# Kernel tuning notes

Measured on AMD Instinct MI355X. Metric: run time of the kernel, lower is better.

The kernel has to match this reference:

```python
import jax, jax.numpy as jnp
import numpy as np

N = 40000
E = 640000
D_IN = 128
D_OUT = 128
K = 3
LAMBDA_MAX = 2.0
LN_EPS = 1e-5


def setup_inputs() -> dict:
    key = jax.random.key(0)
    k1, k2, k3, k4, k5 = jax.random.split(key, 5)
    x = jax.random.normal(k1, (N, D_IN), dtype=jnp.float32)
    edge_index = jax.random.randint(k2, (2, E), 0, N, dtype=jnp.int64)
    edge_weight = jax.random.uniform(k3, (E,), dtype=jnp.float32)
    # Chebyshev weights: one [D_IN, D_OUT] matrix per hop k, plus shared bias
    W = jax.random.normal(k4, (K, D_IN, D_OUT), dtype=jnp.float32) / np.sqrt(D_IN)
    bias = jnp.zeros((D_OUT,), dtype=jnp.float32)
    gamma = jnp.ones((D_OUT,), dtype=jnp.float32)
    beta = jnp.zeros((D_OUT,), dtype=jnp.float32)
    return {"x": x, "edge_weight": edge_weight, "W": W, "bias": bias,
            "gamma": gamma, "beta": beta, "edge_index": edge_index}


def reference(x, edge_weight, W, bias, gamma, beta, edge_index):
    row, col = edge_index[0], edge_index[1]

    # Symmetric normalization of the graph Laplacian (PyG ChebConv, norm='sym')
    deg = jax.ops.segment_sum(edge_weight, row, num_segments=N)
    dinv = jnp.where(deg > 0, jax.lax.rsqrt(deg), 0.0)
    # scaled Laplacian L_hat = (2/lambda_max) * (I - A_norm) - I
    # off-diagonal entries: -(2/lambda_max) * a_norm ; diagonal: 2/lambda_max - 1
    scale = 2.0 / LAMBDA_MAX
    norm = -scale * dinv[row] * edge_weight * dinv[col]  # [E]
    diag = scale - 1.0  # == 0 for lambda_max = 2

    def prop(h):  # L_hat @ h via gather / scale / scatter-add
        msg = norm[:, None] * h[col]                      # [E, D]
        return jax.ops.segment_sum(msg, row, num_segments=N) + diag * h

    # Chebyshev recursion: T0 = x, T1 = L_hat x, Tk = 2 L_hat T_{k-1} - T_{k-2}
    Tx0 = x
    out = Tx0 @ W[0]
    Tx1 = prop(x)
    out = out + Tx1 @ W[1]
    for k in range(2, K):
        Tx2 = 2.0 * prop(Tx1) - Tx0
        out = out + Tx2 @ W[k]
        Tx0, Tx1 = Tx1, Tx2
    out = out + bias

    # LayerNorm over channels + ReLU
    mean = jnp.mean(out, axis=-1, keepdims=True)
    var = jnp.var(out, axis=-1, keepdims=True)
    out = (out - mean) * jax.lax.rsqrt(var + LN_EPS) * gamma + beta
    return jax.nn.relu(out)
```

## Files before the change

### kernel.cpp

```cpp
#include <hip/hip_runtime.h>

#define NN 40000
#define EE 640000
#define DD 128
#define CAP 96

typedef __attribute__((ext_vector_type(8))) __bf16 bf16x8;
typedef __attribute__((ext_vector_type(4))) float f32x4;
typedef unsigned long long ull;

static __device__ __forceinline__ unsigned short bfs(float f) {
    __bf16 h = (__bf16)f;
    return __builtin_bit_cast(unsigned short, h);
}
static __device__ __forceinline__ float blo(unsigned int v) {
    return __builtin_bit_cast(float, v << 16);
}
static __device__ __forceinline__ float bhi(unsigned int v) {
    return __builtin_bit_cast(float, v & 0xffff0000u);
}

__global__ __launch_bounds__(256) void k_pre(const int* __restrict__ ei,
                                             const float* __restrict__ ew,
                                             const float* __restrict__ x,
                                             const float* __restrict__ W,
                                             ull* __restrict__ degcnt,
                                             int2* __restrict__ pair,
                                             unsigned short* __restrict__ xb,
                                             unsigned short* __restrict__ Wt) {
    int b = blockIdx.x;
    int tid = threadIdx.x;
    if (b < 2500) {
        int e = b * 256 + tid;
        int r = ei[e];
        int c = ei[EE + e];
        float w = ew[e];
        unsigned int q = __float2uint_rn(w * 16777216.0f);
        ull old = atomicAdd(degcnt + r, (1ULL << 32) | (ull)q);
        int rk = (int)(old >> 32);
        if (rk < CAP)
            pair[(size_t)r * CAP + rk] = make_int2(c, __float_as_int(w));
    } else if (b < 3125) {
        int base = (b - 2500) * 2048 + tid;
        #pragma unroll
        for (int it = 0; it < 8; it++) {
            int i = base + it * 256;
            float4 v = ((const float4*)x)[i];
            ushort4 p;
            p.x = bfs(v.x); p.y = bfs(v.y); p.z = bfs(v.z); p.w = bfs(v.w);
            ((ushort4*)xb)[i] = p;
        }
    } else {
        int t = (b - 3125) * 256 + tid;
        int n = t / 384;
        int c = t - n * 384;
        Wt[t] = bfs(W[(size_t)c * 128 + n]);
    }
}

__global__ __launch_bounds__(256) void k_dinv(const ull* __restrict__ degcnt,
                                              float* __restrict__ dinv) {
    int i = blockIdx.x * 256 + threadIdx.x;
    if (i < NN) {
        unsigned int lo = (unsigned int)degcnt[i];
        dinv[i] = lo > 0 ? rsqrtf((float)lo * (1.0f / 16777216.0f)) : 0.0f;
    }
}

__global__ __launch_bounds__(256) void k_prop(const ull* __restrict__ degcnt,
                                              const int2* __restrict__ pair,
                                              const unsigned short* __restrict__ hb,
                                              const float* __restrict__ dinv,
                                              const unsigned short* __restrict__ subb,
                                              float alpha, float betac,
                                              unsigned short* __restrict__ outb) {
    int grp = (blockIdx.x * 256 + threadIdx.x) >> 4;
    int q = threadIdx.x & 15;

    ull dc = degcnt[grp];
    int cnt = (int)(dc >> 32);
    if (cnt > CAP) cnt = CAP;
    unsigned int lo = (unsigned int)dc;
    float dr = lo > 0 ? rsqrtf((float)lo * (1.0f / 16777216.0f)) : 0.0f;

    int s = grp * CAP, t = s + cnt;
    float a0 = 0.f, a1 = 0.f, a2 = 0.f, a3 = 0.f, a4 = 0.f, a5 = 0.f, a6 = 0.f, a7 = 0.f;

    int e = s;
    for (; e + 4 <= t; e += 4) {
        int2 p0 = pair[e + 0];
        int2 p1 = pair[e + 1];
        int2 p2 = pair[e + 2];
        int2 p3 = pair[e + 3];
        uint4 h0 = *(const uint4*)(hb + (size_t)p0.x * DD + q * 8);
        uint4 h1 = *(const uint4*)(hb + (size_t)p1.x * DD + q * 8);
        uint4 h2 = *(const uint4*)(hb + (size_t)p2.x * DD + q * 8);
        uint4 h3 = *(const uint4*)(hb + (size_t)p3.x * DD + q * 8);
        float n0 = __int_as_float(p0.y) * dinv[p0.x];
        float n1 = __int_as_float(p1.y) * dinv[p1.x];
        float n2 = __int_as_float(p2.y) * dinv[p2.x];
        float n3 = __int_as_float(p3.y) * dinv[p3.x];
        a0 = fmaf(n0, blo(h0.x), a0); a1 = fmaf(n0, bhi(h0.x), a1);
        a2 = fmaf(n0, blo(h0.y), a2); a3 = fmaf(n0, bhi(h0.y), a3);
        a4 = fmaf(n0, blo(h0.z), a4); a5 = fmaf(n0, bhi(h0.z), a5);
        a6 = fmaf(n0, blo(h0.w), a6); a7 = fmaf(n0, bhi(h0.w), a7);
        a0 = fmaf(n1, blo(h1.x), a0); a1 = fmaf(n1, bhi(h1.x), a1);
        a2 = fmaf(n1, blo(h1.y), a2); a3 = fmaf(n1, bhi(h1.y), a3);
        a4 = fmaf(n1, blo(h1.z), a4); a5 = fmaf(n1, bhi(h1.z), a5);
        a6 = fmaf(n1, blo(h1.w), a6); a7 = fmaf(n1, bhi(h1.w), a7);
        a0 = fmaf(n2, blo(h2.x), a0); a1 = fmaf(n2, bhi(h2.x), a1);
        a2 = fmaf(n2, blo(h2.y), a2); a3 = fmaf(n2, bhi(h2.y), a3);
        a4 = fmaf(n2, blo(h2.z), a4); a5 = fmaf(n2, bhi(h2.z), a5);
        a6 = fmaf(n2, blo(h2.w), a6); a7 = fmaf(n2, bhi(h2.w), a7);
        a0 = fmaf(n3, blo(h3.x), a0); a1 = fmaf(n3, bhi(h3.x), a1);
        a2 = fmaf(n3, blo(h3.y), a2); a3 = fmaf(n3, bhi(h3.y), a3);
        a4 = fmaf(n3, blo(h3.z), a4); a5 = fmaf(n3, bhi(h3.z), a5);
        a6 = fmaf(n3, blo(h3.w), a6); a7 = fmaf(n3, bhi(h3.w), a7);
    }
    for (; e < t; e++) {
        int2 pr = pair[e];
        float nv = __int_as_float(pr.y) * dinv[pr.x];
        uint4 hv = *(const uint4*)(hb + (size_t)pr.x * DD + q * 8);
        a0 = fmaf(nv, blo(hv.x), a0); a1 = fmaf(nv, bhi(hv.x), a1);
        a2 = fmaf(nv, blo(hv.y), a2); a3 = fmaf(nv, bhi(hv.y), a3);
        a4 = fmaf(nv, blo(hv.z), a4); a5 = fmaf(nv, bhi(hv.z), a5);
        a6 = fmaf(nv, blo(hv.w), a6); a7 = fmaf(nv, bhi(hv.w), a7);
    }

    float scale = -alpha * dr;
    if (subb != nullptr) {
        const unsigned short* sp = subb + (size_t)grp * DD + q * 8;
        uint4 sv = *(const uint4*)sp;
        a0 = fmaf(scale, a0, betac * blo(sv.x));
        a1 = fmaf(scale, a1, betac * bhi(sv.x));
        a2 = fmaf(scale, a2, betac * blo(sv.y));
        a3 = fmaf(scale, a3, betac * bhi(sv.y));
        a4 = fmaf(scale, a4, betac * blo(sv.z));
        a5 = fmaf(scale, a5, betac * bhi(sv.z));
        a6 = fmaf(scale, a6, betac * blo(sv.w));
        a7 = fmaf(scale, a7, betac * bhi(sv.w));
    } else {
        a0 *= scale; a1 *= scale; a2 *= scale; a3 *= scale;
        a4 *= scale; a5 *= scale; a6 *= scale; a7 *= scale;
    }
    ushort4 o0, o1;
    o0.x = bfs(a0); o0.y = bfs(a1); o0.z = bfs(a2); o0.w = bfs(a3);
    o1.x = bfs(a4); o1.y = bfs(a5); o1.z = bfs(a6); o1.w = bfs(a7);
    unsigned short* op = outb + (size_t)grp * DD + q * 8;
    *(ushort4*)(op) = o0;
    *(ushort4*)(op + 4) = o1;
}

__global__ __launch_bounds__(256) void k_gemm_mfma_ln(
        const unsigned short* __restrict__ xb, const unsigned short* __restrict__ t1b,
        const unsigned short* __restrict__ t2b, const unsigned short* __restrict__ Wt,
        const float* __restrict__ bias, const float* __restrict__ gamma,
        const float* __restrict__ beta, float* __restrict__ out) {
    int tid = threadIdx.x;
    int lane = tid & 63;
    int wv = tid >> 6;
    int quad = lane >> 4;
    int l15 = lane & 15;
    int rowq = blockIdx.x * 128 + wv * 32;

    int r0 = rowq + l15;       if (r0 > NN - 1) r0 = NN - 1;
    int r1 = rowq + 16 + l15;  if (r1 > NN - 1) r1 = NN - 1;

    float bias_l[8], gamma_l[8], beta_l[8];
    #pragma unroll
    for (int nt = 0; nt < 8; nt++) {
        int cc = nt * 16 + l15;
        bias_l[nt] = bias[cc];
        gamma_l[nt] = gamma[cc];
        beta_l[nt] = beta[cc];
    }

    f32x4 acc[2][8];
    #pragma unroll
    for (int mt = 0; mt < 2; mt++)
        #pragma unroll
        for (int nt = 0; nt < 8; nt++)
            acc[mt][nt] = (f32x4){0.f, 0.f, 0.f, 0.f};

    #pragma unroll
    for (int c = 0; c < 12; c++) {
        const unsigned short* src = (c < 4) ? xb : ((c < 8) ? t1b : t2b);
        int kk = (c & 3) * 32 + quad * 8;
        bf16x8 a0 = *(const bf16x8*)(src + (size_t)r0 * DD + kk);
        bf16x8 a1 = *(const bf16x8*)(src + (size_t)r1 * DD + kk);
        #pragma unroll
        for (int nt = 0; nt < 8; nt++) {
            bf16x8 b = *(const bf16x8*)(Wt + (size_t)(nt * 16 + l15) * 384 + c * 32 + quad * 8);
            acc[0][nt] = __builtin_amdgcn_mfma_f32_16x16x32_bf16(a0, b, acc[0][nt], 0, 0, 0);
            acc[1][nt] = __builtin_amdgcn_mfma_f32_16x16x32_bf16(a1, b, acc[1][nt], 0, 0, 0);
        }
    }

    #pragma unroll
    for (int mt = 0; mt < 2; mt++) {
        #pragma unroll
        for (int reg = 0; reg < 4; reg++) {
            float v[8];
            float s = 0.f, sq = 0.f;
            #pragma unroll
            for (int nt = 0; nt < 8; nt++) {
                v[nt] = acc[mt][nt][reg] + bias_l[nt];
                s += v[nt];
                sq += v[nt] * v[nt];
            }
            #pragma unroll
            for (int m = 1; m <= 8; m <<= 1) {
                s  += __shfl_xor(s, m, 64);
                sq += __shfl_xor(sq, m, 64);
            }
            float mean = s * (1.0f / 128.0f);
            float var = sq * (1.0f / 128.0f) - mean * mean;
            float inv = rsqrtf(var + 1e-5f);
            int grow = rowq + mt * 16 + quad * 4 + reg;
            if (grow < NN) {
                #pragma unroll
                for (int nt = 0; nt < 8; nt++) {
                    float o = fmaxf((v[nt] - mean) * inv * gamma_l[nt] + beta_l[nt], 0.0f);
                    out[(size_t)grow * DD + nt * 16 + l15] = o;
                }
            }
        }
    }
}

extern "C" void kernel_launch(void* const* d_in, const int* in_sizes, int n_in,
                              void* d_out, int out_size, void* d_ws, size_t ws_size,
                              hipStream_t stream) {
    const float* x     = (const float*)d_in[0];
    const float* ew    = (const float*)d_in[1];
    const float* W     = (const float*)d_in[2];
    const float* bias  = (const float*)d_in[3];
    const float* gamma = (const float*)d_in[4];
    const float* beta  = (const float*)d_in[5];
    const int*   ei    = (const int*)d_in[6];
    float* out = (float*)d_out;

    char* ws = (char*)d_ws;
    size_t o = 0;
    auto alloc = [&](size_t bytes) { void* p = ws + o; o += (bytes + 255) & ~(size_t)255; return p; };
    ull*   degcnt = (ull*) alloc((size_t)NN * 8);
    float* dinv  = (float*)alloc((size_t)NN * 4);
    int2*  pair  = (int2*) alloc((size_t)NN * CAP * 8);
    unsigned short* xb  = (unsigned short*)alloc((size_t)NN * DD * 2);
    unsigned short* t1b = (unsigned short*)alloc((size_t)NN * DD * 2);
    unsigned short* t2b = (unsigned short*)alloc((size_t)NN * DD * 2);
    unsigned short* Wt  = (unsigned short*)alloc((size_t)384 * 128 * 2);

    hipMemsetAsync(degcnt, 0, (size_t)NN * 8, stream);

    k_pre<<<3317, 256, 0, stream>>>(ei, ew, x, W, degcnt, pair, xb, Wt);
    k_dinv<<<(NN + 255) / 256, 256, 0, stream>>>(degcnt, dinv);

    k_prop<<<NN / 16, 256, 0, stream>>>(degcnt, pair, xb, dinv, nullptr, 1.0f, 0.0f, t1b);
    k_prop<<<NN / 16, 256, 0, stream>>>(degcnt, pair, t1b, dinv, xb, 2.0f, -1.0f, t2b);

    k_gemm_mfma_ln<<<(NN + 127) / 128, 256, 0, stream>>>(xb, t1b, t2b, Wt, bias, gamma, beta, out);
}
```

Before: 206.0 us.

## Fuse dinv into propagation, batch tail edges, retile GEMM to 160-row blocks

Drops the separate dinv kernel and its buffer. Each propagation step now recomputes rsqrt of the neighbour degree from degcnt on the fly, which removes one launch but does an 8-byte load plus an rsqrt per edge. The scalar remainder loop becomes a single masked batch of three edges, so the gathers can be issued together. The GEMM+LayerNorm kernel uses 5 waves per block over 250 blocks, which divides 40000 rows exactly, so the clamping and bounds checks are removed.

```diff
diff --git a/kernel.cpp b/kernel.cpp
--- a/kernel.cpp
+++ b/kernel.cpp
@@ -18,6 +18,10 @@
 }
 static __device__ __forceinline__ float bhi(unsigned int v) {
     return __builtin_bit_cast(float, v & 0xffff0000u);
+}
+static __device__ __forceinline__ float dinv_of(ull dc) {
+    unsigned int lo = (unsigned int)dc;
+    return lo > 0 ? rsqrtf((float)lo * (1.0f / 16777216.0f)) : 0.0f;
 }
 
 __global__ __launch_bounds__(256) void k_pre(const int* __restrict__ ei,
@@ -58,19 +62,9 @@
     }
 }
 
-__global__ __launch_bounds__(256) void k_dinv(const ull* __restrict__ degcnt,
-                                              float* __restrict__ dinv) {
-    int i = blockIdx.x * 256 + threadIdx.x;
-    if (i < NN) {
-        unsigned int lo = (unsigned int)degcnt[i];
-        dinv[i] = lo > 0 ? rsqrtf((float)lo * (1.0f / 16777216.0f)) : 0.0f;
-    }
-}
-
 __global__ __launch_bounds__(256) void k_prop(const ull* __restrict__ degcnt,
                                               const int2* __restrict__ pair,
                                               const unsigned short* __restrict__ hb,
-                                              const float* __restrict__ dinv,
                                               const unsigned short* __restrict__ subb,
                                               float alpha, float betac,
                                               unsigned short* __restrict__ outb) {
@@ -80,8 +74,7 @@
     ull dc = degcnt[grp];
     int cnt = (int)(dc >> 32);
     if (cnt > CAP) cnt = CAP;
-    unsigned int lo = (unsigned int)dc;
-    float dr = lo > 0 ? rsqrtf((float)lo * (1.0f / 16777216.0f)) : 0.0f;
+    float dr = dinv_of(dc);
 
     int s = grp * CAP, t = s + cnt;
     float a0 = 0.f, a1 = 0.f, a2 = 0.f, a3 = 0.f, a4 = 0.f, a5 = 0.f, a6 = 0.f, a7 = 0.f;
@@ -96,10 +89,10 @@
         uint4 h1 = *(const uint4*)(hb + (size_t)p1.x * DD + q * 8);
         uint4 h2 = *(const uint4*)(hb + (size_t)p2.x * DD + q * 8);
         uint4 h3 = *(const uint4*)(hb + (size_t)p3.x * DD + q * 8);
-        float n0 = __int_as_float(p0.y) * dinv[p0.x];
-        float n1 = __int_as_float(p1.y) * dinv[p1.x];
-        float n2 = __int_as_float(p2.y) * dinv[p2.x];
-        float n3 = __int_as_float(p3.y) * dinv[p3.x];
+        float n0 = __int_as_float(p0.y) * dinv_of(degcnt[p0.x]);
+        float n1 = __int_as_float(p1.y) * dinv_of(degcnt[p1.x]);
+        float n2 = __int_as_float(p2.y) * dinv_of(degcnt[p2.x]);
+        float n3 = __int_as_float(p3.y) * dinv_of(degcnt[p3.x]);
         a0 = fmaf(n0, blo(h0.x), a0); a1 = fmaf(n0, bhi(h0.x), a1);
         a2 = fmaf(n0, blo(h0.y), a2); a3 = fmaf(n0, bhi(h0.y), a3);
         a4 = fmaf(n0, blo(h0.z), a4); a5 = fmaf(n0, bhi(h0.z), a5);
@@ -117,14 +110,32 @@
         a4 = fmaf(n3, blo(h3.z), a4); a5 = fmaf(n3, bhi(h3.z), a5);
         a6 = fmaf(n3, blo(h3.w), a6); a7 = fmaf(n3, bhi(h3.w), a7);
     }
-    for (; e < t; e++) {
-        int2 pr = pair[e];
-        float nv = __int_as_float(pr.y) * dinv[pr.x];
-        uint4 hv = *(const uint4*)(hb + (size_t)pr.x * DD + q * 8);
-        a0 = fmaf(nv, blo(hv.x), a0); a1 = fmaf(nv, bhi(hv.x), a1);
-        a2 = fmaf(nv, blo(hv.y), a2); a3 = fmaf(nv, bhi(hv.y), a3);
-        a4 = fmaf(nv, blo(hv.z), a4); a5 = fmaf(nv, bhi(hv.z), a5);
-        a6 = fmaf(nv, blo(hv.w), a6); a7 = fmaf(nv, bhi(hv.w), a7);
+    if (e < t) {
+        int i1 = (e + 1 < t) ? e + 1 : t - 1;
+        int i2 = (e + 2 < t) ? e + 2 : t - 1;
+        float m1 = (e + 1 < t) ? 1.f : 0.f;
+        float m2 = (e + 2 < t) ? 1.f : 0.f;
+        int2 p0 = pair[e];
+        int2 p1 = pair[i1];
+        int2 p2 = pair[i2];
+        uint4 h0 = *(const uint4*)(hb + (size_t)p0.x * DD + q * 8);
+        uint4 h1 = *(const uint4*)(hb + (size_t)p1.x * DD + q * 8);
+        uint4 h2 = *(const uint4*)(hb + (size_t)p2.x * DD + q * 8);
+        float n0 = __int_as_float(p0.y) * dinv_of(degcnt[p0.x]);
+        float n1 = m1 * __int_as_float(p1.y) * dinv_of(degcnt[p1.x]);
+        float n2 = m2 * __int_as_float(p2.y) * dinv_of(degcnt[p2.x]);
+        a0 = fmaf(n0, blo(h0.x), a0); a1 = fmaf(n0, bhi(h0.x), a1);
+        a2 = fmaf(n0, blo(h0.y), a2); a3 = fmaf(n0, bhi(h0.y), a3);
+        a4 = fmaf(n0, blo(h0.z), a4); a5 = fmaf(n0, bhi(h0.z), a5);
+        a6 = fmaf(n0, blo(h0.w), a6); a7 = fmaf(n0, bhi(h0.w), a7);
+        a0 = fmaf(n1, blo(h1.x), a0); a1 = fmaf(n1, bhi(h1.x), a1);
+        a2 = fmaf(n1, blo(h1.y), a2); a3 = fmaf(n1, bhi(h1.y), a3);
+        a4 = fmaf(n1, blo(h1.z), a4); a5 = fmaf(n1, bhi(h1.z), a5);
+        a6 = fmaf(n1, blo(h1.w), a6); a7 = fmaf(n1, bhi(h1.w), a7);
+        a0 = fmaf(n2, blo(h2.x), a0); a1 = fmaf(n2, bhi(h2.x), a1);
+        a2 = fmaf(n2, blo(h2.y), a2); a3 = fmaf(n2, bhi(h2.y), a3);
+        a4 = fmaf(n2, blo(h2.z), a4); a5 = fmaf(n2, bhi(h2.z), a5);
+        a6 = fmaf(n2, blo(h2.w), a6); a7 = fmaf(n2, bhi(h2.w), a7);
     }
 
     float scale = -alpha * dr;
@@ -151,7 +162,7 @@
     *(ushort4*)(op + 4) = o1;
 }
 
-__global__ __launch_bounds__(256) void k_gemm_mfma_ln(
+__global__ __launch_bounds__(320) void k_gemm_mfma_ln(
         const unsigned short* __restrict__ xb, const unsigned short* __restrict__ t1b,
         const unsigned short* __restrict__ t2b, const unsigned short* __restrict__ Wt,
         const float* __restrict__ bias, const float* __restrict__ gamma,
@@ -161,10 +172,10 @@
     int wv = tid >> 6;
     int quad = lane >> 4;
     int l15 = lane & 15;
-    int rowq = blockIdx.x * 128 + wv * 32;
-
-    int r0 = rowq + l15;       if (r0 > NN - 1) r0 = NN - 1;
-    int r1 = rowq + 16 + l15;  if (r1 > NN - 1) r1 = NN - 1;
+    int rowq = blockIdx.x * 160 + wv * 32;
+
+    int r0 = rowq + l15;
+    int r1 = rowq + 16 + l15;
 
     float bias_l[8], gamma_l[8], beta_l[8];
     #pragma unroll
@@ -217,12 +228,10 @@
             float var = sq * (1.0f / 128.0f) - mean * mean;
             float inv = rsqrtf(var + 1e-5f);
             int grow = rowq + mt * 16 + quad * 4 + reg;
-            if (grow < NN) {
-                #pragma unroll
-                for (int nt = 0; nt < 8; nt++) {
-                    float o = fmaxf((v[nt] - mean) * inv * gamma_l[nt] + beta_l[nt], 0.0f);
-                    out[(size_t)grow * DD + nt * 16 + l15] = o;
-                }
+            #pragma unroll
+            for (int nt = 0; nt < 8; nt++) {
+                float o = fmaxf((v[nt] - mean) * inv * gamma_l[nt] + beta_l[nt], 0.0f);
+                out[(size_t)grow * DD + nt * 16 + l15] = o;
             }
         }
     }
@@ -244,7 +253,6 @@
     size_t o = 0;
     auto alloc = [&](size_t bytes) { void* p = ws + o; o += (bytes + 255) & ~(size_t)255; return p; };
     ull*   degcnt = (ull*) alloc((size_t)NN * 8);
-    float* dinv  = (float*)alloc((size_t)NN * 4);
     int2*  pair  = (int2*) alloc((size_t)NN * CAP * 8);
     unsigned short* xb  = (unsigned short*)alloc((size_t)NN * DD * 2);
     unsigned short* t1b = (unsigned short*)alloc((size_t)NN * DD * 2);
@@ -254,10 +262,9 @@
     hipMemsetAsync(degcnt, 0, (size_t)NN * 8, stream);
 
     k_pre<<<3317, 256, 0, stream>>>(ei, ew, x, W, degcnt, pair, xb, Wt);
-    k_dinv<<<(NN + 255) / 256, 256, 0, stream>>>(degcnt, dinv);
-
-    k_prop<<<NN / 16, 256, 0, stream>>>(degcnt, pair, xb, dinv, nullptr, 1.0f, 0.0f, t1b);
-    k_prop<<<NN / 16, 256, 0, stream>>>(degcnt, pair, t1b, dinv, xb, 2.0f, -1.0f, t2b);
-
-    k_gemm_mfma_ln<<<(NN + 127) / 128, 256, 0, stream>>>(xb, t1b, t2b, Wt, bias, gamma, beta, out);
-}
+
+    k_prop<<<NN / 16, 256, 0, stream>>>(degcnt, pair, xb, nullptr, 1.0f, 0.0f, t1b);
+    k_prop<<<NN / 16, 256, 0, stream>>>(degcnt, pair, t1b, xb, 2.0f, -1.0f, t2b);
+
+    k_gemm_mfma_ln<<<250, 320, 0, stream>>>(xb, t1b, t2b, Wt, bias, gamma, beta, out);
+}
```

After: 212.8 us. +3.3%, slower.
